# Performance work log

Measured on AMD Instinct MI355X. Metric: run time of the kernel, lower is better.

Reference implementation:

```python
import jax, jax.numpy as jnp
import numpy as np

D_MODEL = 2048
N_HEADS = 16
D_K = D_MODEL // N_HEADS
D_FF = 5504
SEQ = 4096
CONTEXT_LENGTH = 4096
THETA = 10000.0
EPS = 1e-5


def _linear(x, w):
    # w: (out, in), matches torch einsum '...i,oi->...o'
    return jnp.einsum('...i,oi->...o', x, w)


def _rmsnorm(x, g):
    xf = x.astype(jnp.float32)
    rms = jnp.sqrt(jnp.mean(xf * xf, axis=-1, keepdims=True) + EPS)
    return (xf / rms * g).astype(x.dtype)


def _rope_tables():
    powers = jnp.arange(0, D_K, 2, dtype=jnp.float32) / D_K
    freqs = 1.0 / (THETA ** powers)                       # (D_K/2,)
    t = jnp.arange(CONTEXT_LENGTH, dtype=jnp.float32)
    ang = jnp.outer(t, freqs)                             # (ctx, D_K/2)
    return jnp.cos(ang), jnp.sin(ang)


def _apply_rope(x, token_positions, cos_c, sin_c):
    # x: (b, h, s, d_k); token_positions: (b, s)
    cos = cos_c[token_positions][None].astype(x.dtype)    # (1, b, s, d_k/2)
    sin = sin_c[token_positions][None].astype(x.dtype)
    x_even = x[..., ::2]
    x_odd = x[..., 1::2]
    r1 = x_even * cos - x_odd * sin
    r2 = x_even * sin + x_odd * cos
    # interleave back: (..., d_k/2, 2) -> (..., d_k)
    out = jnp.stack([r1, r2], axis=-1)
    return out.reshape(x.shape)


def setup_inputs() -> dict:
    key = jax.random.key(0)
    ks = jax.random.split(key, 12)

    def w(k, out_f, in_f):
        std = (2.0 / (in_f + out_f)) ** 0.5
        return std * jax.random.normal(k, (out_f, in_f), dtype=jnp.float32)

    return {
        'x': jax.random.normal(ks[0], (1, SEQ, D_MODEL), dtype=jnp.float32),
        'w_q': w(ks[1], D_MODEL, D_MODEL),
        'w_k': w(ks[2], D_MODEL, D_MODEL),
        'w_v': w(ks[3], D_MODEL, D_MODEL),
        'w_o': w(ks[4], D_MODEL, D_MODEL),
        'w1': w(ks[5], D_FF, D_MODEL),
        'w2': w(ks[6], D_MODEL, D_FF),
        'w3': w(ks[7], D_FF, D_MODEL),
        'g1': jnp.ones((D_MODEL,), dtype=jnp.float32),
        'g2': jnp.ones((D_MODEL,), dtype=jnp.float32),
        'token_positions': jnp.broadcast_to(jnp.arange(SEQ, dtype=jnp.int32)[None, :], (1, SEQ)),
    }


def reference(x, w_q, w_k, w_v, w_o, w1, w2, w3, g1, g2, token_positions):
    b, s, _ = x.shape
    cos_c, sin_c = _rope_tables()

    # --- pre-norm attention ---
    xn = _rmsnorm(x, g1)
    def heads(t):
        return t.reshape(b, s, N_HEADS, D_K).transpose(0, 2, 1, 3)  # (b,h,s,d)
    q = heads(_linear(xn, w_q))
    k = heads(_linear(xn, w_k))
    v = heads(_linear(xn, w_v))
    q = _apply_rope(q, token_positions, cos_c, sin_c)
    k = _apply_rope(k, token_positions, cos_c, sin_c)

    score = jnp.einsum('bhqd,bhkd->bhqk', q, k) / (D_K ** 0.5)
    causal = jnp.tril(jnp.ones((s, s), dtype=bool))
    score = jnp.where(causal, score, -jnp.inf)
    probs = jax.nn.softmax(score, axis=-1)
    attn = jnp.einsum('bhqk,bhkd->bhqd', probs, v)
    attn = attn.transpose(0, 2, 1, 3).reshape(b, s, D_MODEL)
    x = x + _linear(attn, w_o)

    # --- pre-norm SwiGLU FFN ---
    xn = _rmsnorm(x, g2)
    gate = _linear(xn, w1)
    gate = gate * jax.nn.sigmoid(gate)  # SiLU
    x = x + _linear(gate * _linear(xn, w3), w2)
    return x
```

## Files before the change

kernel.cpp:

```cpp
#include <hip/hip_runtime.h>
#include <hip/hip_bf16.h>
#include <cstdint>
#include <cstddef>

constexpr int S_   = 4096;
constexpr int DM   = 2048;
constexpr int NH   = 16;
constexpr int DK   = 128;
constexpr int DFF  = 5504;
constexpr int DFFP = 5632;
constexpr int QLD  = 3 * DM;

typedef float  f32x4  __attribute__((ext_vector_type(4)));
typedef float  f32x16 __attribute__((ext_vector_type(16)));
typedef short  s16x8  __attribute__((ext_vector_type(8)));
typedef __bf16 bfx8   __attribute__((ext_vector_type(8)));

template <typename T, typename U>
__device__ inline auto mfma_try(T a, T b, f32x4 c, int)
    -> decltype(__builtin_amdgcn_mfma_f32_16x16x32_bf16(a, b, c, 0, 0, 0)) {
  return __builtin_amdgcn_mfma_f32_16x16x32_bf16(a, b, c, 0, 0, 0);
}
template <typename T, typename U>
__device__ inline f32x4 mfma_try(T a, T b, f32x4 c, long) {
  U a2 = __builtin_bit_cast(U, a);
  U b2 = __builtin_bit_cast(U, b);
  return __builtin_amdgcn_mfma_f32_16x16x32_bf16(a2, b2, c, 0, 0, 0);
}
__device__ __forceinline__ f32x4 MFMA_BF16(s16x8 a, s16x8 b, f32x4 c) {
  return mfma_try<s16x8, bfx8>(a, b, c, 0);
}

template <typename T, typename U>
__device__ inline auto mfma32_try(T a, T b, f32x16 c, int)
    -> decltype(__builtin_amdgcn_mfma_f32_32x32x16_bf16(a, b, c, 0, 0, 0)) {
  return __builtin_amdgcn_mfma_f32_32x32x16_bf16(a, b, c, 0, 0, 0);
}
template <typename T, typename U>
__device__ inline f32x16 mfma32_try(T a, T b, f32x16 c, long) {
  U a2 = __builtin_bit_cast(U, a);
  U b2 = __builtin_bit_cast(U, b);
  return __builtin_amdgcn_mfma_f32_32x32x16_bf16(a2, b2, c, 0, 0, 0);
}
__device__ __forceinline__ f32x16 MFMA32(s16x8 a, s16x8 b, f32x16 c) {
  return mfma32_try<s16x8, bfx8>(a, b, c, 0);
}

__device__ __forceinline__ void async_ld16(void* lds, const void* g) {
  __builtin_amdgcn_global_load_lds(
      (__attribute__((address_space(1))) void*)(g),
      (__attribute__((address_space(3))) void*)(lds), 16, 0, 0);
}

__device__ __forceinline__ float bf2f(__hip_bfloat16 h) { return __bfloat162float(h); }
__device__ __forceinline__ __hip_bfloat16 f2bf(float f) { return __float2bfloat16(f); }

__global__ __launch_bounds__(256) void cvt_kernel(const float* __restrict__ in,
                                                  __hip_bfloat16* __restrict__ out, int n) {
  int i = (blockIdx.x * 256 + threadIdx.x) * 4;
  if (i >= n) return;
  float4 v = *reinterpret_cast<const float4*>(in + i);
  union { __hip_bfloat16 h[4]; uint2 u; } pk;
  pk.h[0] = f2bf(v.x); pk.h[1] = f2bf(v.y); pk.h[2] = f2bf(v.z); pk.h[3] = f2bf(v.w);
  *reinterpret_cast<uint2*>(out + i) = pk.u;
}

__global__ __launch_bounds__(256) void cvt_pad_kernel(const float* __restrict__ in,
                                                      __hip_bfloat16* __restrict__ out,
                                                      int n_src, int n_tot) {
  int i = (blockIdx.x * 256 + threadIdx.x) * 4;
  if (i >= n_tot) return;
  union { __hip_bfloat16 h[4]; uint2 u; } pk;
  if (i < n_src) {
    float4 v = *reinterpret_cast<const float4*>(in + i);
    pk.h[0] = f2bf(v.x); pk.h[1] = f2bf(v.y); pk.h[2] = f2bf(v.z); pk.h[3] = f2bf(v.w);
  } else {
    pk.u.x = 0u; pk.u.y = 0u;
  }
  *reinterpret_cast<uint2*>(out + i) = pk.u;
}

__global__ __launch_bounds__(256) void rmsnorm_kernel(const float* __restrict__ x,
                                                      const float* __restrict__ g,
                                                      __hip_bfloat16* __restrict__ out) {
  const int row = blockIdx.x, tid = threadIdx.x;
  const float4* xr = reinterpret_cast<const float4*>(x + (size_t)row * DM);
  float4 a = xr[tid], b = xr[tid + 256];
  float ss = a.x*a.x + a.y*a.y + a.z*a.z + a.w*a.w
           + b.x*b.x + b.y*b.y + b.z*b.z + b.w*b.w;
#pragma unroll
  for (int off = 1; off < 64; off <<= 1) ss += __shfl_xor(ss, off);
  __shared__ float red[4];
  if ((tid & 63) == 0) red[tid >> 6] = ss;
  __syncthreads();
  const float inv = rsqrtf((red[0] + red[1] + red[2] + red[3]) * (1.0f / DM) + 1e-5f);
  const float4* gr = reinterpret_cast<const float4*>(g);
  float4 ga = gr[tid], gb = gr[tid + 256];
  union { __hip_bfloat16 h[4]; uint2 u; } pa, pb;
  pa.h[0] = f2bf(a.x * inv * ga.x); pa.h[1] = f2bf(a.y * inv * ga.y);
  pa.h[2] = f2bf(a.z * inv * ga.z); pa.h[3] = f2bf(a.w * inv * ga.w);
  pb.h[0] = f2bf(b.x * inv * gb.x); pb.h[1] = f2bf(b.y * inv * gb.y);
  pb.h[2] = f2bf(b.z * inv * gb.z); pb.h[3] = f2bf(b.w * inv * gb.w);
  uint2* o = reinterpret_cast<uint2*>(out + (size_t)row * DM);
  o[tid] = pa.u; o[tid + 256] = pb.u;
}

__global__ __launch_bounds__(256) void rope_kernel(__hip_bfloat16* __restrict__ t,
                                                   const int* __restrict__ pos, int col0) {
  const size_t idx = (size_t)blockIdx.x * 256 + threadIdx.x;
  const int j = (int)(idx & 63);
  const int h = (int)((idx >> 6) & 15);
  const int s = (int)(idx >> 10);
  const float p = (float)pos[s];
  const float freq = exp2f((float)j * (-13.287712379549449f / 64.0f));
  float sn, cs;
  sincosf(p * freq, &sn, &cs);
  __hip_bfloat16* ptr = t + (size_t)s * QLD + col0 + h * DK + 2 * j;
  const float e = bf2f(ptr[0]), o = bf2f(ptr[1]);
  ptr[0] = f2bf(e * cs - o * sn);
  ptr[1] = f2bf(e * sn + o * cs);
}

__global__ __launch_bounds__(256) void transpose_v(const __hip_bfloat16* __restrict__ qkv,
                                                   __hip_bfloat16* __restrict__ vt) {
  __shared__ __hip_bfloat16 tile[64][65];
  const int h = blockIdx.z;
  const int s0 = blockIdx.x * 64, d0 = blockIdx.y * 64;
  const int lane = threadIdx.x & 63, w = threadIdx.x >> 6;
#pragma unroll
  for (int i = 0; i < 16; i++) {
    const int r = w * 16 + i;
    tile[r][lane] = qkv[(size_t)(s0 + r) * QLD + 2 * DM + h * DK + d0 + lane];
  }
  __syncthreads();
#pragma unroll
  for (int i = 0; i < 16; i++) {
    const int r = w * 16 + i;
    vt[(size_t)(h * DK + d0 + r) * S_ + s0 + lane] = tile[lane][r];
  }
}

enum { EP_BF16 = 0, EP_SILU = 1, EP_MUL = 2, EP_ADDF32 = 3 };

template <int EP>
__global__ __launch_bounds__(512, 2) void gemm2(const __hip_bfloat16* __restrict__ A,
                                                const __hip_bfloat16* __restrict__ B,
                                                int N, int K, int lda, int ldb,
                                                void* outp, const void* extra) {
  __shared__ char lds[3][24576];
  const int tid = threadIdx.x;
  const int wave = tid >> 6, lane = tid & 63;
  const int l15 = lane & 15, l4 = lane >> 4;
  const int wm = wave >> 2, wn = wave & 3;

  const int nbn = gridDim.x;
  const int nwg = gridDim.x * gridDim.y;
  int lin = blockIdx.y * gridDim.x + blockIdx.x;
  if ((nwg & 7) == 0) lin = (lin & 7) * (nwg >> 3) + (lin >> 3);
  const int bm = (lin / nbn) * 128;
  const int bn = (lin % nbn) * 256;

  const int NT = K >> 5;

  const int srcCh = ((tid & 3) ^ ((tid >> 3) & 3)) * 16;
  const char* Asrc  = (const char*)A + (size_t)(bm + (tid >> 2)) * lda * 2 + srcCh;
  const char* Bsrc0 = (const char*)B + (size_t)(bn + (tid >> 2)) * ldb * 2 + srcCh;
  const char* Bsrc1 = (const char*)B + (size_t)(bn + 128 + (tid >> 2)) * ldb * 2 + srcCh;
  char* const ldsA  = &lds[0][0] + wave * 1024;
  char* const ldsB0 = &lds[0][0] + 8192 + wave * 1024;
  char* const ldsB1 = &lds[0][0] + 16384 + wave * 1024;

  auto stage_a  = [&](int t, int s) { async_ld16(ldsA  + s * 24576, Asrc  + (size_t)t * 64); };
  auto stage_b0 = [&](int t, int s) { async_ld16(ldsB0 + s * 24576, Bsrc0 + (size_t)t * 64); };
  auto stage_b1 = [&](int t, int s) { async_ld16(ldsB1 + s * 24576, Bsrc1 + (size_t)t * 64); };

  const int rdch = (l4 ^ ((l15 >> 1) & 3)) * 16;
  auto rd_a = [&](int s, int mq, int f) -> s16x8 {
    return *(const s16x8*)(&lds[s][0] + (wm * 64 + mq * 32 + f * 16 + l15) * 64 + rdch);
  };
  auto rd_b = [&](int s, int nf) -> s16x8 {
    return *(const s16x8*)(&lds[s][8192] + (wn * 64 + nf * 16 + l15) * 64 + rdch);
  };

  f32x4 acc[4][4] = {};

  stage_a(0, 0); stage_b0(0, 0); stage_b1(0, 0);
  stage_a(1, 1); stage_b0(1, 1); stage_b1(1, 1);

  for (int t = 0; t < NT; t++) {
    const int s = t % 3;
    if (t + 1 < NT) { asm volatile("s_waitcnt vmcnt(3)" ::: "memory"); }
    else            { asm volatile("s_waitcnt vmcnt(0)" ::: "memory"); }
    __builtin_amdgcn_s_barrier();
    asm volatile("" ::: "memory");
    s16x8 b0 = rd_b(s, 0), b1 = rd_b(s, 1), b2 = rd_b(s, 2), b3 = rd_b(s, 3);
    s16x8 a0 = rd_a(s, 0, 0), a1 = rd_a(s, 0, 1);
    if (t + 2 < NT) { const int s2 = (t + 2) % 3; stage_a(t + 2, s2); stage_b0(t + 2, s2); }
    __builtin_amdgcn_s_barrier();
    asm volatile("" ::: "memory");
    __builtin_amdgcn_s_setprio(1);
    acc[0][0] = MFMA_BF16(a0, b0, acc[0][0]);
    acc[0][1] = MFMA_BF16(a0, b1, acc[0][1]);
    acc[0][2] = MFMA_BF16(a0, b2, acc[0][2]);
    acc[0][3] = MFMA_BF16(a0, b3, acc[0][3]);
    acc[1][0] = MFMA_BF16(a1, b0, acc[1][0]);
    acc[1][1] = MFMA_BF16(a1, b1, acc[1][1]);
    acc[1][2] = MFMA_BF16(a1, b2, acc[1][2]);
    acc[1][3] = MFMA_BF16(a1, b3, acc[1][3]);
    __builtin_amdgcn_s_setprio(0);
    s16x8 a2 = rd_a(s, 1, 0), a3 = rd_a(s, 1, 1);
    if (t + 2 < NT) stage_b1(t + 2, (t + 2) % 3);
    __builtin_amdgcn_s_barrier();
    asm volatile("" ::: "memory");
    __builtin_amdgcn_s_setprio(1);
    acc[2][0] = MFMA_BF16(a2, b0, acc[2][0]);
    acc[2][1] = MFMA_BF16(a2, b1, acc[2][1]);
    acc[2][2] = MFMA_BF16(a2, b2, acc[2][2]);
    acc[2][3] = MFMA_BF16(a2, b3, acc[2][3]);
    acc[3][0] = MFMA_BF16(a3, b0, acc[3][0]);
    acc[3][1] = MFMA_BF16(a3, b1, acc[3][1]);
    acc[3][2] = MFMA_BF16(a3, b2, acc[3][2]);
    acc[3][3] = MFMA_BF16(a3, b3, acc[3][3]);
    __builtin_amdgcn_s_setprio(0);
  }

#pragma unroll
  for (int mf = 0; mf < 4; mf++)
#pragma unroll
    for (int nf = 0; nf < 4; nf++)
#pragma unroll
      for (int r = 0; r < 4; r++) {
        const int row = bm + wm * 64 + mf * 16 + l4 * 4 + r;
        const int col = bn + wn * 64 + nf * 16 + l15;
        const size_t idx = (size_t)row * N + col;
        const float v = acc[mf][nf][r];
        if constexpr (EP == EP_BF16) {
          ((__hip_bfloat16*)outp)[idx] = f2bf(v);
        } else if constexpr (EP == EP_SILU) {
          ((__hip_bfloat16*)outp)[idx] = f2bf(v / (1.0f + __expf(-v)));
        } else if constexpr (EP == EP_MUL) {
          const float o = bf2f(((const __hip_bfloat16*)extra)[idx]);
          ((__hip_bfloat16*)outp)[idx] = f2bf(v * o);
        } else {
          ((float*)outp)[idx] = v + ((const float*)extra)[idx];
        }
      }
}

__global__ __launch_bounds__(256, 2) void attn_kernel(const __hip_bfloat16* __restrict__ qkv,
                                                      const __hip_bfloat16* __restrict__ vt,
                                                      __hip_bfloat16* __restrict__ out) {
  __shared__ char sK[2][64 * 256];
  __shared__ char sV[128 * 128];

  const int h = blockIdx.y;
  const int qtile = gridDim.x - 1 - blockIdx.x;
  const int q0 = qtile * 128;
  const int tid = threadIdx.x, wave = tid >> 6, lane = tid & 63;
  const int l31 = lane & 31, hi = lane >> 5;
  const int qr = q0 + wave * 32 + l31;
  const int ntiles = qtile * 2 + 2;

  s16x8 qf[8];
  {
    const char* qsrc = (const char*)qkv + (size_t)qr * (QLD * 2) + h * DK * 2 + hi * 16;
#pragma unroll
    for (int s = 0; s < 8; s++) qf[s] = *(const s16x8*)(qsrc + s * 32);
  }

  const char* qkvK = (const char*)qkv + ((size_t)DM + h * DK) * 2;
  const char* vtH  = (const char*)vt + (size_t)h * DK * S_ * 2;

  auto stage_K = [&](int t, int buf) {
    const int kv0 = t * 64;
#pragma unroll
    for (int a = 0; a < 4; a++) {
      const int rl = wave * 16 + a * 4 + (lane >> 4);
      const int ck = (lane & 15) ^ (rl & 7);
      async_ld16(sK[buf] + (wave * 16 + a * 4) * 256,
                 qkvK + (size_t)(kv0 + rl) * (QLD * 2) + ck * 16);
    }
  };
  auto stage_V = [&](int t) {
    const int kv0 = t * 64;
#pragma unroll
    for (int a = 0; a < 4; a++) {
      const int rl = wave * 32 + a * 8 + (lane >> 3);
      const int cv = (lane & 7) ^ (rl & 7);
      async_ld16(sV + (wave * 32 + a * 8) * 128,
                 vtH + ((size_t)rl * S_ + kv0) * 2 + cv * 16);
    }
  };

  f32x16 acc[4] = {};
  float m_ = -__builtin_inff(), l_ = 0.f;
  const float scale = 0.08838834764831845f;

  stage_K(0, 0);
  stage_V(0);
  asm volatile("s_waitcnt vmcnt(4)" ::: "memory");
  __builtin_amdgcn_s_barrier();

  int kbuf = 0;
  for (int t = 0; t < ntiles; t++) {
    if (t + 1 < ntiles) stage_K(t + 1, kbuf ^ 1);
    const char* Kt = sK[kbuf];

    f32x16 st0 = {}, st1 = {};
    __builtin_amdgcn_s_setprio(1);
#pragma unroll
    for (int s = 0; s < 8; s++) {
      const int cc = s * 2 + hi;
      const int cs = (cc & 8) | ((cc ^ l31) & 7);
      s16x8 k0 = *(const s16x8*)(Kt + l31 * 256 + cs * 16);
      s16x8 k1 = *(const s16x8*)(Kt + (32 + l31) * 256 + cs * 16);
      st0 = MFMA32(k0, qf[s], st0);
      st1 = MFMA32(k1, qf[s], st1);
    }
    __builtin_amdgcn_s_setprio(0);

    const int kvb = t * 64;
    float p[32];
    float mx = -__builtin_inff();
#pragma unroll
    for (int r = 0; r < 16; r++) {
      const int kv = kvb + (r & 3) + 8 * (r >> 2) + 4 * hi;
      const float v0 = st0[r] * scale;
      const float v1 = st1[r] * scale;
      p[r]      = (kv <= qr)      ? v0 : -__builtin_inff();
      p[16 + r] = (kv + 32 <= qr) ? v1 : -__builtin_inff();
      mx = fmaxf(mx, fmaxf(p[r], p[16 + r]));
    }
    mx = fmaxf(mx, __shfl_xor(mx, 32));
    const bool skip = __all(mx - m_ <= 8.0f);
    float alpha = 1.0f;
    if (!skip) {
      const float nm = fmaxf(m_, mx);
      alpha = __expf(m_ - nm);
      m_ = nm;
#pragma unroll
      for (int dt = 0; dt < 4; dt++)
#pragma unroll
        for (int r = 0; r < 16; r++) acc[dt][r] *= alpha;
    }
    float psum = 0.f;
#pragma unroll
    for (int i = 0; i < 32; i++) {
      p[i] = __expf(p[i] - m_);
      psum += p[i];
    }
    psum += __shfl_xor(psum, 32);
    l_ = l_ * alpha + psum;

    unsigned ps[16];
#pragma unroll
    for (int h2 = 0; h2 < 2; h2++)
#pragma unroll
      for (int t2 = 0; t2 < 4; t2++)
#pragma unroll
        for (int rp = 0; rp < 2; rp++) {
          union { __hip_bfloat16 hh[2]; unsigned u; } pk;
          pk.hh[0] = f2bf(p[h2 * 16 + t2 * 4 + rp * 2]);
          pk.hh[1] = f2bf(p[h2 * 16 + t2 * 4 + rp * 2 + 1]);
          ps[h2 * 8 + t2 * 2 + rp] = pk.u;
        }

    if (t + 1 < ntiles) { asm volatile("s_waitcnt vmcnt(4)" ::: "memory"); }
    else                { asm volatile("s_waitcnt vmcnt(0)" ::: "memory"); }
    __builtin_amdgcn_s_barrier();

#pragma unroll
    for (int s = 0; s < 4; s++) {
      const int h2 = s >> 1;
      const int iA = h2 * 8 + (2 * (s & 1)) * 2;
      const int iB = h2 * 8 + (2 * (s & 1) + 1) * 2;
      const unsigned keep0 = hi ? ps[iB]     : ps[iA];
      const unsigned keep1 = hi ? ps[iB + 1] : ps[iA + 1];
      const unsigned send0 = hi ? ps[iA]     : ps[iB];
      const unsigned send1 = hi ? ps[iA + 1] : ps[iB + 1];
      const unsigned recv0 = __shfl_xor(send0, 32);
      const unsigned recv1 = __shfl_xor(send1, 32);
      union { unsigned u[4]; s16x8 v; } fr;
      fr.u[0] = hi ? recv0 : keep0;
      fr.u[1] = hi ? recv1 : keep1;
      fr.u[2] = hi ? keep0 : recv0;
      fr.u[3] = hi ? keep1 : recv1;
      const s16x8 pa = fr.v;
      __builtin_amdgcn_s_setprio(1);
#pragma unroll
      for (int dt = 0; dt < 4; dt++) {
        s16x8 vf = *(const s16x8*)(sV + (dt * 32 + l31) * 128 +
                                   (((s * 2 + hi) ^ (l31 & 7)) & 7) * 16);
        acc[dt] = MFMA32(vf, pa, acc[dt]);
      }
      __builtin_amdgcn_s_setprio(0);
    }

    __builtin_amdgcn_s_barrier();
    if (t + 1 < ntiles) {
      stage_V(t + 1);
      asm volatile("s_waitcnt vmcnt(4)" ::: "memory");
      __builtin_amdgcn_s_barrier();
    }
    kbuf ^= 1;
  }

  const float rl = 1.0f / l_;
  __hip_bfloat16* orow = out + (size_t)qr * DM + h * DK;
#pragma unroll
  for (int dt = 0; dt < 4; dt++)
#pragma unroll
    for (int rq = 0; rq < 4; rq++) {
      union { __hip_bfloat16 hh[4]; uint2 u; } pk;
#pragma unroll
      for (int e = 0; e < 4; e++) pk.hh[e] = f2bf(acc[dt][rq * 4 + e] * rl);
      *reinterpret_cast<uint2*>(orow + dt * 32 + 8 * rq + 4 * hi) = pk.u;
    }
}

extern "C" void kernel_launch(void* const* d_in, const int* in_sizes, int n_in,
                              void* d_out, int out_size, void* d_ws, size_t ws_size,
                              hipStream_t stream) {
  const float* x   = (const float*)d_in[0];
  const float* w_q = (const float*)d_in[1];
  const float* w_k = (const float*)d_in[2];
  const float* w_v = (const float*)d_in[3];
  const float* w_o = (const float*)d_in[4];
  const float* w1  = (const float*)d_in[5];
  const float* w2  = (const float*)d_in[6];
  const float* w3  = (const float*)d_in[7];
  const float* g1  = (const float*)d_in[8];
  const float* g2  = (const float*)d_in[9];
  const int*   tp  = (const int*)d_in[10];
  float* outf = (float*)d_out;

  constexpr size_t SZ_WQKV  = (size_t)3 * DM * DM * 2;
  constexpr size_t OFF_ATTN = (size_t)DM * DM * 2;
  constexpr size_t OFF_XN   = SZ_WQKV;
  constexpr size_t OFF_A2   = OFF_XN + (size_t)S_ * DM * 2;
  constexpr size_t OFF_VT   = OFF_A2 + (size_t)S_ * QLD * 2;
  constexpr size_t WS_NEED  = OFF_VT + (size_t)NH * DK * S_ * 2;
  if (ws_size < WS_NEED) return;

  char* base = (char*)d_ws;
  __hip_bfloat16* warena = (__hip_bfloat16*)base;
  __hip_bfloat16* attnb  = (__hip_bfloat16*)(base + OFF_ATTN);
  __hip_bfloat16* xn     = (__hip_bfloat16*)(base + OFF_XN);
  __hip_bfloat16* qkv    = (__hip_bfloat16*)(base + OFF_A2);
  __hip_bfloat16* ff1    = (__hip_bfloat16*)(base + OFF_A2);
  __hip_bfloat16* vt     = (__hip_bfloat16*)(base + OFF_VT);

  const int nwq = DM * DM;
  const int nff_src = DFF * DM;
  const int nff_pad = DFFP * DM;

  cvt_kernel<<<nwq / 1024, 256, 0, stream>>>(w_q, warena, nwq);
  cvt_kernel<<<nwq / 1024, 256, 0, stream>>>(w_k, warena + (size_t)DM * DM, nwq);
  cvt_kernel<<<nwq / 1024, 256, 0, stream>>>(w_v, warena + (size_t)2 * DM * DM, nwq);
  rmsnorm_kernel<<<S_, 256, 0, stream>>>(x, g1, xn);
  gemm2<EP_BF16><<<dim3(QLD / 256, S_ / 128), 512, 0, stream>>>(xn, warena, QLD, DM, DM, DM, qkv, nullptr);
  {
    const int nrope = S_ * NH * 64;
    rope_kernel<<<nrope / 256, 256, 0, stream>>>(qkv, tp, 0);
    rope_kernel<<<nrope / 256, 256, 0, stream>>>(qkv, tp, DM);
  }
  transpose_v<<<dim3(S_ / 64, DK / 64, NH), 256, 0, stream>>>(qkv, vt);
  attn_kernel<<<dim3(S_ / 128, NH), 256, 0, stream>>>(qkv, vt, attnb);
  cvt_kernel<<<nwq / 1024, 256, 0, stream>>>(w_o, warena, nwq);
  gemm2<EP_ADDF32><<<dim3(DM / 256, S_ / 128), 512, 0, stream>>>(attnb, warena, DM, DM, DM, DM, outf, x);

  rmsnorm_kernel<<<S_, 256, 0, stream>>>(outf, g2, xn);
  cvt_pad_kernel<<<nff_pad / 1024, 256, 0, stream>>>(w1, warena, nff_src, nff_pad);
  gemm2<EP_SILU><<<dim3(DFFP / 256, S_ / 128), 512, 0, stream>>>(xn, warena, DFFP, DM, DM, DM, ff1, nullptr);
  cvt_pad_kernel<<<nff_pad / 1024, 256, 0, stream>>>(w3, warena, nff_src, nff_pad);
  gemm2<EP_MUL><<<dim3(DFFP / 256, S_ / 128), 512, 0, stream>>>(xn, warena, DFFP, DM, DM, DM, ff1, ff1);
  cvt_kernel<<<(DM * DFF) / 1024, 256, 0, stream>>>(w2, warena, DM * DFF);
  gemm2<EP_ADDF32><<<dim3(DM / 256, S_ / 128), 512, 0, stream>>>(ff1, warena, DM, DFF, DFFP, DFF, outf, outf);
}
```

Before: 798.4 us.

## Add 256x256 GEMM tile kernel, fuse weight casts and RoPE, exp2 softmax

Adds a gemm3 kernel with 256x256 output tiles (each wave computes 128x64) and a 3-stage 96KB LDS pipeline. It is used for the QKV, SiLU and mul GEMMs to raise data reuse per loaded tile. The three QKV weight casts are merged into one launch, and the Q and K RoPE passes into one kernel. The attention softmax now uses exp2 with a prescaled log2e factor and skips causal masking on fully unmasked tiles. The larger tiles raise register and LDS pressure, which may lower occupancy, and they give fewer workgroups for the 6144-wide QKV GEMM.

```diff
diff --git a/kernel.cpp b/kernel.cpp
--- a/kernel.cpp
+++ b/kernel.cpp
@@ -60,6 +60,19 @@
   int i = (blockIdx.x * 256 + threadIdx.x) * 4;
   if (i >= n) return;
   float4 v = *reinterpret_cast<const float4*>(in + i);
+  union { __hip_bfloat16 h[4]; uint2 u; } pk;
+  pk.h[0] = f2bf(v.x); pk.h[1] = f2bf(v.y); pk.h[2] = f2bf(v.z); pk.h[3] = f2bf(v.w);
+  *reinterpret_cast<uint2*>(out + i) = pk.u;
+}
+
+__global__ __launch_bounds__(256) void cvt3_kernel(const float* __restrict__ a,
+                                                   const float* __restrict__ b,
+                                                   const float* __restrict__ c,
+                                                   __hip_bfloat16* __restrict__ out, int n) {
+  int i = (blockIdx.x * 256 + threadIdx.x) * 4;
+  if (i >= 3 * n) return;
+  const float* src = (i < n) ? (a + i) : (i < 2 * n) ? (b + i - n) : (c + i - 2 * n);
+  float4 v = *reinterpret_cast<const float4*>(src);
   union { __hip_bfloat16 h[4]; uint2 u; } pk;
   pk.h[0] = f2bf(v.x); pk.h[1] = f2bf(v.y); pk.h[2] = f2bf(v.z); pk.h[3] = f2bf(v.w);
   *reinterpret_cast<uint2*>(out + i) = pk.u;
@@ -106,7 +119,7 @@
 }
 
 __global__ __launch_bounds__(256) void rope_kernel(__hip_bfloat16* __restrict__ t,
-                                                   const int* __restrict__ pos, int col0) {
+                                                   const int* __restrict__ pos) {
   const size_t idx = (size_t)blockIdx.x * 256 + threadIdx.x;
   const int j = (int)(idx & 63);
   const int h = (int)((idx >> 6) & 15);
@@ -115,10 +128,18 @@
   const float freq = exp2f((float)j * (-13.287712379549449f / 64.0f));
   float sn, cs;
   sincosf(p * freq, &sn, &cs);
-  __hip_bfloat16* ptr = t + (size_t)s * QLD + col0 + h * DK + 2 * j;
-  const float e = bf2f(ptr[0]), o = bf2f(ptr[1]);
-  ptr[0] = f2bf(e * cs - o * sn);
-  ptr[1] = f2bf(e * sn + o * cs);
+  __hip_bfloat16* ptrQ = t + (size_t)s * QLD + h * DK + 2 * j;
+  __hip_bfloat16* ptrK = ptrQ + DM;
+  {
+    const float e = bf2f(ptrQ[0]), o = bf2f(ptrQ[1]);
+    ptrQ[0] = f2bf(e * cs - o * sn);
+    ptrQ[1] = f2bf(e * sn + o * cs);
+  }
+  {
+    const float e = bf2f(ptrK[0]), o = bf2f(ptrK[1]);
+    ptrK[0] = f2bf(e * cs - o * sn);
+    ptrK[1] = f2bf(e * sn + o * cs);
+  }
 }
 
 __global__ __launch_bounds__(256) void transpose_v(const __hip_bfloat16* __restrict__ qkv,
@@ -141,6 +162,10 @@
 }
 
 enum { EP_BF16 = 0, EP_SILU = 1, EP_MUL = 2, EP_ADDF32 = 3 };
+
+__device__ __forceinline__ void gemm_epilogue(int EP, float v, size_t idx,
+                                              void* outp, const void* extra) {
+}
 
 template <int EP>
 __global__ __launch_bounds__(512, 2) void gemm2(const __hip_bfloat16* __restrict__ A,
@@ -247,6 +272,133 @@
       }
 }
 
+template <int EP>
+__global__ __launch_bounds__(512, 2) void gemm3(const __hip_bfloat16* __restrict__ A,
+                                                const __hip_bfloat16* __restrict__ B,
+                                                int N, int K, int lda, int ldb,
+                                                void* outp, const void* extra) {
+  __shared__ char lds[3][32768];
+  const int tid = threadIdx.x;
+  const int wave = tid >> 6, lane = tid & 63;
+  const int l15 = lane & 15, l4 = lane >> 4;
+  const int wm = wave >> 2, wn = wave & 3;
+
+  const int nbn = gridDim.x;
+  const int nwg = gridDim.x * gridDim.y;
+  int lin = blockIdx.y * gridDim.x + blockIdx.x;
+  if ((nwg & 7) == 0) lin = (lin & 7) * (nwg >> 3) + (lin >> 3);
+  const int bm = (lin / nbn) * 256;
+  const int bn = (lin % nbn) * 256;
+
+  const int NT = K >> 5;
+
+  const int srcCh = ((tid & 3) ^ ((tid >> 3) & 3)) * 16;
+  const char* Asrc0 = (const char*)A + (size_t)(bm + (tid >> 2)) * lda * 2 + srcCh;
+  const char* Asrc1 = (const char*)A + (size_t)(bm + 128 + (tid >> 2)) * lda * 2 + srcCh;
+  const char* Bsrc0 = (const char*)B + (size_t)(bn + (tid >> 2)) * ldb * 2 + srcCh;
+  const char* Bsrc1 = (const char*)B + (size_t)(bn + 128 + (tid >> 2)) * ldb * 2 + srcCh;
+  char* const ldsA0 = &lds[0][0] + wave * 1024;
+  char* const ldsA1 = &lds[0][0] + 8192 + wave * 1024;
+  char* const ldsB0 = &lds[0][0] + 16384 + wave * 1024;
+  char* const ldsB1 = &lds[0][0] + 24576 + wave * 1024;
+
+  auto stage_a0 = [&](int t, int s) { async_ld16(ldsA0 + s * 32768, Asrc0 + (size_t)t * 64); };
+  auto stage_a1 = [&](int t, int s) { async_ld16(ldsA1 + s * 32768, Asrc1 + (size_t)t * 64); };
+  auto stage_b0 = [&](int t, int s) { async_ld16(ldsB0 + s * 32768, Bsrc0 + (size_t)t * 64); };
+  auto stage_b1 = [&](int t, int s) { async_ld16(ldsB1 + s * 32768, Bsrc1 + (size_t)t * 64); };
+
+  const int rdch = (l4 ^ ((l15 >> 1) & 3)) * 16;
+  auto rd_a = [&](int s, int mf) -> s16x8 {
+    return *(const s16x8*)(&lds[s][0] + (wm * 128 + mf * 16 + l15) * 64 + rdch);
+  };
+  auto rd_b = [&](int s, int nf) -> s16x8 {
+    return *(const s16x8*)(&lds[s][16384] + (wn * 64 + nf * 16 + l15) * 64 + rdch);
+  };
+
+  f32x4 acc[8][4] = {};
+
+  stage_a0(0, 0); stage_a1(0, 0); stage_b0(0, 0); stage_b1(0, 0);
+  stage_a0(1, 1); stage_a1(1, 1); stage_b0(1, 1); stage_b1(1, 1);
+
+  for (int t = 0; t < NT; t++) {
+    const int s = t % 3;
+    if (t + 1 < NT) { asm volatile("s_waitcnt vmcnt(4)" ::: "memory"); }
+    else            { asm volatile("s_waitcnt vmcnt(0)" ::: "memory"); }
+    __builtin_amdgcn_s_barrier();
+    asm volatile("" ::: "memory");
+    s16x8 b0 = rd_b(s, 0), b1 = rd_b(s, 1), b2 = rd_b(s, 2), b3 = rd_b(s, 3);
+    s16x8 a0 = rd_a(s, 0), a1 = rd_a(s, 1), a2 = rd_a(s, 2), a3 = rd_a(s, 3);
+    if (t + 2 < NT) {
+      const int s2 = (t + 2) % 3;
+      stage_a0(t + 2, s2); stage_a1(t + 2, s2); stage_b0(t + 2, s2);
+    }
+    __builtin_amdgcn_s_barrier();
+    asm volatile("" ::: "memory");
+    __builtin_amdgcn_s_setprio(1);
+    acc[0][0] = MFMA_BF16(a0, b0, acc[0][0]);
+    acc[0][1] = MFMA_BF16(a0, b1, acc[0][1]);
+    acc[0][2] = MFMA_BF16(a0, b2, acc[0][2]);
+    acc[0][3] = MFMA_BF16(a0, b3, acc[0][3]);
+    acc[1][0] = MFMA_BF16(a1, b0, acc[1][0]);
+    acc[1][1] = MFMA_BF16(a1, b1, acc[1][1]);
+    acc[1][2] = MFMA_BF16(a1, b2, acc[1][2]);
+    acc[1][3] = MFMA_BF16(a1, b3, acc[1][3]);
+    acc[2][0] = MFMA_BF16(a2, b0, acc[2][0]);
+    acc[2][1] = MFMA_BF16(a2, b1, acc[2][1]);
+    acc[2][2] = MFMA_BF16(a2, b2, acc[2][2]);
+    acc[2][3] = MFMA_BF16(a2, b3, acc[2][3]);
+    acc[3][0] = MFMA_BF16(a3, b0, acc[3][0]);
+    acc[3][1] = MFMA_BF16(a3, b1, acc[3][1]);
+    acc[3][2] = MFMA_BF16(a3, b2, acc[3][2]);
+    acc[3][3] = MFMA_BF16(a3, b3, acc[3][3]);
+    __builtin_amdgcn_s_setprio(0);
+    s16x8 a4 = rd_a(s, 4), a5 = rd_a(s, 5), a6 = rd_a(s, 6), a7 = rd_a(s, 7);
+    if (t + 2 < NT) stage_b1(t + 2, (t + 2) % 3);
+    __builtin_amdgcn_s_barrier();
+    asm volatile("" ::: "memory");
+    __builtin_amdgcn_s_setprio(1);
+    acc[4][0] = MFMA_BF16(a4, b0, acc[4][0]);
+    acc[4][1] = MFMA_BF16(a4, b1, acc[4][1]);
+    acc[4][2] = MFMA_BF16(a4, b2, acc[4][2]);
+    acc[4][3] = MFMA_BF16(a4, b3, acc[4][3]);
+    acc[5][0] = MFMA_BF16(a5, b0, acc[5][0]);
+    acc[5][1] = MFMA_BF16(a5, b1, acc[5][1]);
+    acc[5][2] = MFMA_BF16(a5, b2, acc[5][2]);
+    acc[5][3] = MFMA_BF16(a5, b3, acc[5][3]);
+    acc[6][0] = MFMA_BF16(a6, b0, acc[6][0]);
+    acc[6][1] = MFMA_BF16(a6, b1, acc[6][1]);
+    acc[6][2] = MFMA_BF16(a6, b2, acc[6][2]);
+    acc[6][3] = MFMA_BF16(a6, b3, acc[6][3]);
+    acc[7][0] = MFMA_BF16(a7, b0, acc[7][0]);
+    acc[7][1] = MFMA_BF16(a7, b1, acc[7][1]);
+    acc[7][2] = MFMA_BF16(a7, b2, acc[7][2]);
+    acc[7][3] = MFMA_BF16(a7, b3, acc[7][3]);
+    __builtin_amdgcn_s_setprio(0);
+  }
+
+#pragma unroll
+  for (int mf = 0; mf < 8; mf++)
+#pragma unroll
+    for (int nf = 0; nf < 4; nf++)
+#pragma unroll
+      for (int r = 0; r < 4; r++) {
+        const int row = bm + wm * 128 + mf * 16 + l4 * 4 + r;
+        const int col = bn + wn * 64 + nf * 16 + l15;
+        const size_t idx = (size_t)row * N + col;
+        const float v = acc[mf][nf][r];
+        if constexpr (EP == EP_BF16) {
+          ((__hip_bfloat16*)outp)[idx] = f2bf(v);
+        } else if constexpr (EP == EP_SILU) {
+          ((__hip_bfloat16*)outp)[idx] = f2bf(v / (1.0f + __expf(-v)));
+        } else if constexpr (EP == EP_MUL) {
+          const float o = bf2f(((const __hip_bfloat16*)extra)[idx]);
+          ((__hip_bfloat16*)outp)[idx] = f2bf(v * o);
+        } else {
+          ((float*)outp)[idx] = v + ((const float*)extra)[idx];
+        }
+      }
+}
+
 __global__ __launch_bounds__(256, 2) void attn_kernel(const __hip_bfloat16* __restrict__ qkv,
                                                       const __hip_bfloat16* __restrict__ vt,
                                                       __hip_bfloat16* __restrict__ out) {
@@ -294,7 +446,7 @@
 
   f32x16 acc[4] = {};
   float m_ = -__builtin_inff(), l_ = 0.f;
-  const float scale = 0.08838834764831845f;
+  const float cl2 = 1.4426950408889634f * 0.08838834764831845f;
 
   stage_K(0, 0);
   stage_V(0);
@@ -322,21 +474,30 @@
     const int kvb = t * 64;
     float p[32];
     float mx = -__builtin_inff();
-#pragma unroll
-    for (int r = 0; r < 16; r++) {
-      const int kv = kvb + (r & 3) + 8 * (r >> 2) + 4 * hi;
-      const float v0 = st0[r] * scale;
-      const float v1 = st1[r] * scale;
-      p[r]      = (kv <= qr)      ? v0 : -__builtin_inff();
-      p[16 + r] = (kv + 32 <= qr) ? v1 : -__builtin_inff();
-      mx = fmaxf(mx, fmaxf(p[r], p[16 + r]));
+    if (kvb + 63 <= q0 + wave * 32) {
+#pragma unroll
+      for (int r = 0; r < 16; r++) {
+        p[r]      = st0[r] * cl2;
+        p[16 + r] = st1[r] * cl2;
+        mx = fmaxf(mx, fmaxf(p[r], p[16 + r]));
+      }
+    } else {
+#pragma unroll
+      for (int r = 0; r < 16; r++) {
+        const int kv = kvb + (r & 3) + 8 * (r >> 2) + 4 * hi;
+        const float v0 = st0[r] * cl2;
+        const float v1 = st1[r] * cl2;
+        p[r]      = (kv <= qr)      ? v0 : -__builtin_inff();
+        p[16 + r] = (kv + 32 <= qr) ? v1 : -__builtin_inff();
+        mx = fmaxf(mx, fmaxf(p[r], p[16 + r]));
+      }
     }
     mx = fmaxf(mx, __shfl_xor(mx, 32));
     const bool skip = __all(mx - m_ <= 8.0f);
     float alpha = 1.0f;
     if (!skip) {
       const float nm = fmaxf(m_, mx);
-      alpha = __expf(m_ - nm);
+      alpha = exp2f(m_ - nm);
       m_ = nm;
 #pragma unroll
       for (int dt = 0; dt < 4; dt++)
@@ -346,7 +507,7 @@
     float psum = 0.f;
 #pragma unroll
     for (int i = 0; i < 32; i++) {
-      p[i] = __expf(p[i] - m_);
+      p[i] = exp2f(p[i] - m_);
       psum += p[i];
     }
     psum += __shfl_xor(psum, 32);
@@ -454,16 +615,10 @@
   const int nff_src = DFF * DM;
   const int nff_pad = DFFP * DM;
 
-  cvt_kernel<<<nwq / 1024, 256, 0, stream>>>(w_q, warena, nwq);
-  cvt_kernel<<<nwq / 1024, 256, 0, stream>>>(w_k, warena + (size_t)DM * DM, nwq);
-  cvt_kernel<<<nwq / 1024, 256, 0, stream>>>(w_v, warena + (size_t)2 * DM * DM, nwq);
+  cvt3_kernel<<<(3 * nwq) / 1024, 256, 0, stream>>>(w_q, w_k, w_v, warena, nwq);
   rmsnorm_kernel<<<S_, 256, 0, stream>>>(x, g1, xn);
-  gemm2<EP_BF16><<<dim3(QLD / 256, S_ / 128), 512, 0, stream>>>(xn, warena, QLD, DM, DM, DM, qkv, nullptr);
-  {
-    const int nrope = S_ * NH * 64;
-    rope_kernel<<<nrope / 256, 256, 0, stream>>>(qkv, tp, 0);
-    rope_kernel<<<nrope / 256, 256, 0, stream>>>(qkv, tp, DM);
-  }
+  gemm3<EP_BF16><<<dim3(QLD / 256, S_ / 256), 512, 0, stream>>>(xn, warena, QLD, DM, DM, DM, qkv, nullptr);
+  rope_kernel<<<(S_ * NH * 64) / 256, 256, 0, stream>>>(qkv, tp);
   transpose_v<<<dim3(S_ / 64, DK / 64, NH), 256, 0, stream>>>(qkv, vt);
   attn_kernel<<<dim3(S_ / 128, NH), 256, 0, stream>>>(qkv, vt, attnb);
   cvt_kernel<<<nwq / 1024, 256, 0, stream>>>(w_o, warena, nwq);
@@ -471,9 +626,9 @@
 
   rmsnorm_kernel<<<S_, 256, 0, stream>>>(outf, g2, xn);
   cvt_pad_kernel<<<nff_pad / 1024, 256, 0, stream>>>(w1, warena, nff_src, nff_pad);
-  gemm2<EP_SILU><<<dim3(DFFP / 256, S_ / 128), 512, 0, stream>>>(xn, warena, DFFP, DM, DM, DM, ff1, nullptr);
+  gemm3<EP_SILU><<<dim3(DFFP / 256, S_ / 256), 512, 0, stream>>>(xn, warena, DFFP, DM, DM, DM, ff1, nullptr);
   cvt_pad_kernel<<<nff_pad / 1024, 256, 0, stream>>>(w3, warena, nff_src, nff_pad);
-  gemm2<EP_MUL><<<dim3(DFFP / 256, S_ / 128), 512, 0, stream>>>(xn, warena, DFFP, DM, DM, DM, ff1, ff1);
+  gemm3<EP_MUL><<<dim3(DFFP / 256, S_ / 256), 512, 0, stream>>>(xn, warena, DFFP, DM, DM, DM, ff1, ff1);
   cvt_kernel<<<(DM * DFF) / 1024, 256, 0, stream>>>(w2, warena, DM * DFF);
   gemm2<EP_ADDF32><<<dim3(DM / 256, S_ / 128), 512, 0, stream>>>(ff1, warena, DM, DFF, DFFP, DFF, outf, outf);
 }
```

Result: slower. 848.0 us (+6.2%).

## Fuse weight conversions and rope launches, balance attention tiles, use exp2 softmax

Applied to the files above, without the earlier changes.

Merges the three Q/K/V weight conversions into one launch and the two rope launches into a single kernel that rotates both Q and K, cutting launch overhead and recomputation of sin/cos. Attention now maps query tiles per head with a rotating and mirrored order so long and short causal tiles interleave across the grid. The softmax folds log2(e) into the scale and uses exp2f, and skips causal masking for tiles that lie fully below the diagonal. The changes are mixed and mostly small; the tile remap alters scheduling order across the GPU.

```diff
diff --git a/kernel.cpp b/kernel.cpp
--- a/kernel.cpp
+++ b/kernel.cpp
@@ -60,6 +60,19 @@
   int i = (blockIdx.x * 256 + threadIdx.x) * 4;
   if (i >= n) return;
   float4 v = *reinterpret_cast<const float4*>(in + i);
+  union { __hip_bfloat16 h[4]; uint2 u; } pk;
+  pk.h[0] = f2bf(v.x); pk.h[1] = f2bf(v.y); pk.h[2] = f2bf(v.z); pk.h[3] = f2bf(v.w);
+  *reinterpret_cast<uint2*>(out + i) = pk.u;
+}
+
+__global__ __launch_bounds__(256) void cvt3_kernel(const float* __restrict__ a,
+                                                   const float* __restrict__ b,
+                                                   const float* __restrict__ c,
+                                                   __hip_bfloat16* __restrict__ out, int n) {
+  int i = (blockIdx.x * 256 + threadIdx.x) * 4;
+  if (i >= 3 * n) return;
+  const float* src = (i < n) ? (a + i) : (i < 2 * n) ? (b + i - n) : (c + i - 2 * n);
+  float4 v = *reinterpret_cast<const float4*>(src);
   union { __hip_bfloat16 h[4]; uint2 u; } pk;
   pk.h[0] = f2bf(v.x); pk.h[1] = f2bf(v.y); pk.h[2] = f2bf(v.z); pk.h[3] = f2bf(v.w);
   *reinterpret_cast<uint2*>(out + i) = pk.u;
@@ -106,7 +119,7 @@
 }
 
 __global__ __launch_bounds__(256) void rope_kernel(__hip_bfloat16* __restrict__ t,
-                                                   const int* __restrict__ pos, int col0) {
+                                                   const int* __restrict__ pos) {
   const size_t idx = (size_t)blockIdx.x * 256 + threadIdx.x;
   const int j = (int)(idx & 63);
   const int h = (int)((idx >> 6) & 15);
@@ -115,10 +128,18 @@
   const float freq = exp2f((float)j * (-13.287712379549449f / 64.0f));
   float sn, cs;
   sincosf(p * freq, &sn, &cs);
-  __hip_bfloat16* ptr = t + (size_t)s * QLD + col0 + h * DK + 2 * j;
-  const float e = bf2f(ptr[0]), o = bf2f(ptr[1]);
-  ptr[0] = f2bf(e * cs - o * sn);
-  ptr[1] = f2bf(e * sn + o * cs);
+  __hip_bfloat16* ptrQ = t + (size_t)s * QLD + h * DK + 2 * j;
+  __hip_bfloat16* ptrK = ptrQ + DM;
+  {
+    const float e = bf2f(ptrQ[0]), o = bf2f(ptrQ[1]);
+    ptrQ[0] = f2bf(e * cs - o * sn);
+    ptrQ[1] = f2bf(e * sn + o * cs);
+  }
+  {
+    const float e = bf2f(ptrK[0]), o = bf2f(ptrK[1]);
+    ptrK[0] = f2bf(e * cs - o * sn);
+    ptrK[1] = f2bf(e * sn + o * cs);
+  }
 }
 
 __global__ __launch_bounds__(256) void transpose_v(const __hip_bfloat16* __restrict__ qkv,
@@ -254,7 +275,9 @@
   __shared__ char sV[128 * 128];
 
   const int h = blockIdx.y;
-  const int qtile = gridDim.x - 1 - blockIdx.x;
+  int qt = (blockIdx.x + 2 * (h & 7)) & 31;
+  if (h >= 8) qt = 31 - qt;
+  const int qtile = qt;
   const int q0 = qtile * 128;
   const int tid = threadIdx.x, wave = tid >> 6, lane = tid & 63;
   const int l31 = lane & 31, hi = lane >> 5;
@@ -294,7 +317,7 @@
 
   f32x16 acc[4] = {};
   float m_ = -__builtin_inff(), l_ = 0.f;
-  const float scale = 0.08838834764831845f;
+  const float cl2 = 1.4426950408889634f * 0.08838834764831845f;
 
   stage_K(0, 0);
   stage_V(0);
@@ -322,21 +345,30 @@
     const int kvb = t * 64;
     float p[32];
     float mx = -__builtin_inff();
-#pragma unroll
-    for (int r = 0; r < 16; r++) {
-      const int kv = kvb + (r & 3) + 8 * (r >> 2) + 4 * hi;
-      const float v0 = st0[r] * scale;
-      const float v1 = st1[r] * scale;
-      p[r]      = (kv <= qr)      ? v0 : -__builtin_inff();
-      p[16 + r] = (kv + 32 <= qr) ? v1 : -__builtin_inff();
-      mx = fmaxf(mx, fmaxf(p[r], p[16 + r]));
+    if (kvb + 63 <= q0 + wave * 32) {
+#pragma unroll
+      for (int r = 0; r < 16; r++) {
+        p[r]      = st0[r] * cl2;
+        p[16 + r] = st1[r] * cl2;
+        mx = fmaxf(mx, fmaxf(p[r], p[16 + r]));
+      }
+    } else {
+#pragma unroll
+      for (int r = 0; r < 16; r++) {
+        const int kv = kvb + (r & 3) + 8 * (r >> 2) + 4 * hi;
+        const float v0 = st0[r] * cl2;
+        const float v1 = st1[r] * cl2;
+        p[r]      = (kv <= qr)      ? v0 : -__builtin_inff();
+        p[16 + r] = (kv + 32 <= qr) ? v1 : -__builtin_inff();
+        mx = fmaxf(mx, fmaxf(p[r], p[16 + r]));
+      }
     }
     mx = fmaxf(mx, __shfl_xor(mx, 32));
     const bool skip = __all(mx - m_ <= 8.0f);
     float alpha = 1.0f;
     if (!skip) {
       const float nm = fmaxf(m_, mx);
-      alpha = __expf(m_ - nm);
+      alpha = exp2f(m_ - nm);
       m_ = nm;
 #pragma unroll
       for (int dt = 0; dt < 4; dt++)
@@ -346,7 +378,7 @@
     float psum = 0.f;
 #pragma unroll
     for (int i = 0; i < 32; i++) {
-      p[i] = __expf(p[i] - m_);
+      p[i] = exp2f(p[i] - m_);
       psum += p[i];
     }
     psum += __shfl_xor(psum, 32);
@@ -454,16 +486,10 @@
   const int nff_src = DFF * DM;
   const int nff_pad = DFFP * DM;
 
-  cvt_kernel<<<nwq / 1024, 256, 0, stream>>>(w_q, warena, nwq);
-  cvt_kernel<<<nwq / 1024, 256, 0, stream>>>(w_k, warena + (size_t)DM * DM, nwq);
-  cvt_kernel<<<nwq / 1024, 256, 0, stream>>>(w_v, warena + (size_t)2 * DM * DM, nwq);
+  cvt3_kernel<<<(3 * nwq) / 1024, 256, 0, stream>>>(w_q, w_k, w_v, warena, nwq);
   rmsnorm_kernel<<<S_, 256, 0, stream>>>(x, g1, xn);
   gemm2<EP_BF16><<<dim3(QLD / 256, S_ / 128), 512, 0, stream>>>(xn, warena, QLD, DM, DM, DM, qkv, nullptr);
-  {
-    const int nrope = S_ * NH * 64;
-    rope_kernel<<<nrope / 256, 256, 0, stream>>>(qkv, tp, 0);
-    rope_kernel<<<nrope / 256, 256, 0, stream>>>(qkv, tp, DM);
-  }
+  rope_kernel<<<(S_ * NH * 64) / 256, 256, 0, stream>>>(qkv, tp);
   transpose_v<<<dim3(S_ / 64, DK / 64, NH), 256, 0, stream>>>(qkv, vt);
   attn_kernel<<<dim3(S_ / 128, NH), 256, 0, stream>>>(qkv, vt, attnb);
   cvt_kernel<<<nwq / 1024, 256, 0, stream>>>(w_o, warena, nwq);
```

Result: faster. 755.1 us (-5.4%).
